# Performance work log

Hardware: AMD Instinct MI355X
Metric: run time of the kernel (lower is better)

The kernel has to match this reference:

```python
import jax, jax.numpy as jnp
import numpy as np

B, S, D_MODEL, N_HEADS, D_HEAD = 2, 2048, 2048, 16, 128


def _rope_tables(seq_len, d_head, base=10000.0):
    # standard llama RoPE cos/sin tables, broadcastable to (B, H, S, d_head)
    inv_freq = 1.0 / (base ** (np.arange(0, d_head, 2, dtype=np.float32) / d_head))
    t = np.arange(seq_len, dtype=np.float32)
    freqs = np.outer(t, inv_freq)                      # (S, d_head/2)
    emb = np.concatenate([freqs, freqs], axis=-1)       # (S, d_head)
    cos = jnp.asarray(np.cos(emb))[None, None]          # (1,1,S,d_head)
    sin = jnp.asarray(np.sin(emb))[None, None]
    return cos, sin


def setup_inputs() -> dict:
    key = jax.random.key(0)
    ks = jax.random.split(key, 5)
    scale = 0.02
    x = jax.random.normal(ks[0], (B, S, D_MODEL), dtype=jnp.float32)
    Wq = jax.random.normal(ks[1], (D_MODEL, D_MODEL), dtype=jnp.float32) * scale
    Wk = jax.random.normal(ks[2], (D_MODEL, D_MODEL), dtype=jnp.float32) * scale
    Wv = jax.random.normal(ks[3], (D_MODEL, D_MODEL), dtype=jnp.float32) * scale
    Wo = jax.random.normal(ks[4], (D_MODEL, D_MODEL), dtype=jnp.float32) * scale
    cos, sin = _rope_tables(S, D_HEAD)
    return {"x": x, "cos": cos, "sin": sin, "Wq": Wq, "Wk": Wk, "Wv": Wv, "Wo": Wo}


def _rotate_half(x):
    x1, x2 = jnp.split(x, 2, axis=-1)
    return jnp.concatenate([-x2, x1], axis=-1)


def _apply_rope(x, cos, sin):
    return x * cos + _rotate_half(x) * sin


def reference(x, cos, sin, Wq, Wk, Wv, Wo):
    b, s, _ = x.shape
    # QKV projections (nn.Linear computes x @ W.T), reshape to (B, H, S, Dh)
    def proj(W):
        return (x @ W.T).reshape(b, s, N_HEADS, D_HEAD).transpose(0, 2, 1, 3)
    q = _apply_rope(proj(Wq), cos, sin)
    k = _apply_rope(proj(Wk), cos, sin)
    v = proj(Wv)
    # causal scaled dot-product attention
    scale = 1.0 / jnp.sqrt(jnp.asarray(D_HEAD, dtype=x.dtype))
    scores = jnp.einsum("bhqd,bhkd->bhqk", q, k) * scale
    causal = jnp.tril(jnp.ones((s, s), dtype=bool))
    scores = jnp.where(causal, scores, jnp.asarray(-jnp.inf, dtype=scores.dtype))
    attn = jax.nn.softmax(scores, axis=-1)
    vals = jnp.einsum("bhqk,bhkd->bhqd", attn, v)
    vals = vals.transpose(0, 2, 1, 3).reshape(b, s, D_MODEL)
    return vals @ Wo.T
```

## Files before the change

### kernel.cpp

```cpp
#include <hip/hip_runtime.h>

#define S_LEN 2048
#define DMODEL 2048
#define NHEADS 16
#define DHEAD 128
#define BATCH 2

typedef unsigned short u16;
typedef __attribute__((ext_vector_type(8))) __bf16 bf16x8;
typedef __attribute__((ext_vector_type(4))) float f32x4;

__device__ __forceinline__ u16 f2bf(float f) {
    union { float f; unsigned int u; } a; a.f = f;
    unsigned int u = a.u;
    u += 0x7fffu + ((u >> 16) & 1u);
    return (u16)(u >> 16);
}
__device__ __forceinline__ u16 f2bf_fast(float f) {
    union { float f; unsigned int u; } a; a.f = f;
    return (u16)((a.u + 0x8000u) >> 16);
}
__device__ __forceinline__ float bf2f(u16 b) {
    union { unsigned int u; float f; } a; a.u = ((unsigned int)b) << 16;
    return a.f;
}

__device__ __forceinline__ void g2l16(const void* g, void* l) {
    __builtin_amdgcn_global_load_lds((const __attribute__((address_space(1))) unsigned int*)g,
                                     (__attribute__((address_space(3))) unsigned int*)l,
                                     16, 0, 0);
}

__global__ void cvt_all(const float* __restrict__ x,
                        const float* __restrict__ w0, const float* __restrict__ w1,
                        const float* __restrict__ w2, const float* __restrict__ w3,
                        u16* __restrict__ xb, u16* __restrict__ wdst) {
    int y = blockIdx.y;
    const float* src;
    u16* out;
    int n4;
    if (y == 0) { src = x; out = xb; n4 = (BATCH * S_LEN * DMODEL) / 4; }
    else {
        src = (y == 1) ? w0 : (y == 2) ? w1 : (y == 3) ? w2 : w3;
        out = wdst + (size_t)(y - 1) * DMODEL * DMODEL;
        n4 = (DMODEL * DMODEL) / 4;
    }
    int i = blockIdx.x * 256 + threadIdx.x;
    if (i >= n4) return;
    f32x4 v = *(const f32x4*)(src + (size_t)i * 4);
    ushort4 o;
    o.x = f2bf(v[0]); o.y = f2bf(v[1]); o.z = f2bf(v[2]); o.w = f2bf(v[3]);
    *(ushort4*)(out + (size_t)i * 4) = o;
}

#define QK_PRESCALE 0.12751744f
__global__ void rope_kernel(u16* __restrict__ Q, u16* __restrict__ K,
                            const float* __restrict__ cosT, const float* __restrict__ sinT) {
    u16* T = blockIdx.z ? K : Q;
    const float pre = blockIdx.z ? 1.0f : QK_PRESCALE;
    int bh = blockIdx.y;
    int t = blockIdx.x * 256 + threadIdx.x;
    int s = t >> 4;
    int d4 = (t & 15) * 4;
    u16* row = T + ((size_t)bh * S_LEN + s) * DHEAD;
    ushort4 lo = *(ushort4*)&row[d4];
    ushort4 hi = *(ushort4*)&row[d4 + 64];
    f32x4 cv = *(const f32x4*)&cosT[s * DHEAD + d4];
    f32x4 sv = *(const f32x4*)&sinT[s * DHEAD + d4];
    float l0 = bf2f(lo.x), l1 = bf2f(lo.y), l2 = bf2f(lo.z), l3 = bf2f(lo.w);
    float h0 = bf2f(hi.x), h1 = bf2f(hi.y), h2 = bf2f(hi.z), h3 = bf2f(hi.w);
    ushort4 olo, ohi;
    olo.x = f2bf((l0 * cv[0] - h0 * sv[0]) * pre);
    olo.y = f2bf((l1 * cv[1] - h1 * sv[1]) * pre);
    olo.z = f2bf((l2 * cv[2] - h2 * sv[2]) * pre);
    olo.w = f2bf((l3 * cv[3] - h3 * sv[3]) * pre);
    ohi.x = f2bf((h0 * cv[0] + l0 * sv[0]) * pre);
    ohi.y = f2bf((h1 * cv[1] + l1 * sv[1]) * pre);
    ohi.z = f2bf((h2 * cv[2] + l2 * sv[2]) * pre);
    ohi.w = f2bf((h3 * cv[3] + l3 * sv[3]) * pre);
    *(ushort4*)&row[d4]      = olo;
    *(ushort4*)&row[d4 + 64] = ohi;
}

__global__ __launch_bounds__(256) void gemm_qkv(const u16* __restrict__ A,
                                                const u16* __restrict__ W,
                                                u16* __restrict__ Qo,
                                                u16* __restrict__ Ko,
                                                u16* __restrict__ Vto) {
    __shared__ u16 As[128 * 32];
    __shared__ u16 Ws[128 * 32];
    const int tid  = threadIdx.x;
    const int lane = tid & 63;
    const int wave = tid >> 6;
    const int wm = wave >> 1, wn = wave & 1;
    const int col = lane & 15, quad = lane >> 4;
    const int blk = blockIdx.x;
    const int xcd = blk & 7;
    const int loc = blk >> 3;
    const int nb  = xcd * 6 + loc % 6;
    const int mb  = loc / 6;
    const int m0 = mb * 128, n0 = nb * 128;
    const int K = DMODEL;
    const int which = n0 >> 11;

    const u16* P0 = (which == 2) ? A : W;
    const u16* P1 = (which == 2) ? W : A;
    const int  r0 = (which == 2) ? m0 : n0;
    const int  r1 = (which == 2) ? n0 : m0;

    f32x4 acc[4][4] = {};

    const int swl = (quad ^ ((col >> 1) & 3)) * 8;
    int a_off[4], w_off[4];
    #pragma unroll
    for (int mi = 0; mi < 4; ++mi) a_off[mi] = (wm * 64 + mi * 16 + col) * 32 + swl;
    #pragma unroll
    for (int ni = 0; ni < 4; ++ni) w_off[ni] = (wn * 64 + ni * 16 + col) * 32 + swl;

    for (int kk = 0; kk < K; kk += 32) {
        #pragma unroll
        for (int i = 0; i < 2; ++i) {
            int c = i * 256 + tid;
            int row = c >> 2;
            int ko = (((c & 3) ^ ((c >> 3) & 3))) * 8;
            int cb = i * 256 + wave * 64;
            g2l16(P0 + (size_t)(r0 + row) * K + kk + ko, (void*)(As + cb * 8));
            g2l16(P1 + (size_t)(r1 + row) * K + kk + ko, (void*)(Ws + cb * 8));
        }
        __syncthreads();
        bf16x8 af[4], wf[4];
        #pragma unroll
        for (int mi = 0; mi < 4; ++mi) af[mi] = *(const bf16x8*)&As[a_off[mi]];
        #pragma unroll
        for (int ni = 0; ni < 4; ++ni) wf[ni] = *(const bf16x8*)&Ws[w_off[ni]];
        #pragma unroll
        for (int mi = 0; mi < 4; ++mi)
            #pragma unroll
            for (int ni = 0; ni < 4; ++ni)
                acc[mi][ni] = __builtin_amdgcn_mfma_f32_16x16x32_bf16(af[mi], wf[ni], acc[mi][ni], 0, 0, 0);
        __syncthreads();
    }

    if (which == 2) {
        #pragma unroll
        for (int mi = 0; mi < 4; ++mi) {
            #pragma unroll
            for (int ni = 0; ni < 4; ++ni) {
                int s0   = m0 + wm * 64 + mi * 16 + quad * 4;
                int ncol = (n0 & 2047) + wn * 64 + ni * 16 + col;
                int b = s0 >> 11, s = s0 & 2047;
                int h = ncol >> 7, d = ncol & 127;
                ushort4 o;
                o.x = f2bf(acc[mi][ni][0]); o.y = f2bf(acc[mi][ni][1]);
                o.z = f2bf(acc[mi][ni][2]); o.w = f2bf(acc[mi][ni][3]);
                *(ushort4*)&Vto[(((size_t)(b * NHEADS + h)) * DHEAD + d) * S_LEN + s] = o;
            }
        }
    } else {
        u16* out = which ? Ko : Qo;
        #pragma unroll
        for (int mi = 0; mi < 4; ++mi) {
            #pragma unroll
            for (int ni = 0; ni < 4; ++ni) {
                int dd = (n0 & 2047) + wm * 64 + mi * 16 + quad * 4;
                int sg = m0 + wn * 64 + ni * 16 + col;
                int b = sg >> 11, s = sg & 2047;
                int h = dd >> 7, d = dd & 127;
                ushort4 o;
                o.x = f2bf(acc[mi][ni][0]); o.y = f2bf(acc[mi][ni][1]);
                o.z = f2bf(acc[mi][ni][2]); o.w = f2bf(acc[mi][ni][3]);
                *(ushort4*)&out[(((size_t)(b * NHEADS + h)) * S_LEN + s) * DHEAD + d] = o;
            }
        }
    }
}

__global__ __launch_bounds__(256) void gemm_out(const u16* __restrict__ A,
                                                const u16* __restrict__ W,
                                                float* __restrict__ out) {
    __shared__ u16 As[128 * 32];
    __shared__ u16 Ws[128 * 32];
    const int tid  = threadIdx.x;
    const int lane = tid & 63;
    const int wave = tid >> 6;
    const int wm = wave >> 1, wn = wave & 1;
    const int col = lane & 15, quad = lane >> 4;
    const int blk = blockIdx.x;
    const int xcd = blk & 7;
    const int loc = blk >> 3;
    const int nb  = xcd * 2 + (loc & 1);
    const int mb  = loc >> 1;
    const int m0 = mb * 128, n0 = nb * 128;
    const int K = DMODEL;

    f32x4 acc[4][4] = {};

    const int swl = (quad ^ ((col >> 1) & 3)) * 8;
    int a_off[4], w_off[4];
    #pragma unroll
    for (int mi = 0; mi < 4; ++mi) a_off[mi] = (wm * 64 + mi * 16 + col) * 32 + swl;
    #pragma unroll
    for (int ni = 0; ni < 4; ++ni) w_off[ni] = (wn * 64 + ni * 16 + col) * 32 + swl;

    for (int kk = 0; kk < K; kk += 32) {
        #pragma unroll
        for (int i = 0; i < 2; ++i) {
            int c = i * 256 + tid;
            int row = c >> 2;
            int ko = (((c & 3) ^ ((c >> 3) & 3))) * 8;
            int cb = i * 256 + wave * 64;
            g2l16(A + (size_t)(m0 + row) * K + kk + ko, (void*)(As + cb * 8));
            g2l16(W + (size_t)(n0 + row) * K + kk + ko, (void*)(Ws + cb * 8));
        }
        __syncthreads();
        bf16x8 af[4], wf[4];
        #pragma unroll
        for (int mi = 0; mi < 4; ++mi) af[mi] = *(const bf16x8*)&As[a_off[mi]];
        #pragma unroll
        for (int ni = 0; ni < 4; ++ni) wf[ni] = *(const bf16x8*)&Ws[w_off[ni]];
        #pragma unroll
        for (int mi = 0; mi < 4; ++mi)
            #pragma unroll
            for (int ni = 0; ni < 4; ++ni)
                acc[mi][ni] = __builtin_amdgcn_mfma_f32_16x16x32_bf16(af[mi], wf[ni], acc[mi][ni], 0, 0, 0);
        __syncthreads();
    }

    #pragma unroll
    for (int mi = 0; mi < 4; ++mi)
        #pragma unroll
        for (int ni = 0; ni < 4; ++ni)
            #pragma unroll
            for (int r = 0; r < 4; ++r) {
                int row  = m0 + wm * 64 + mi * 16 + quad * 4 + r;
                int ncol = n0 + wn * 64 + ni * 16 + col;
                out[(size_t)row * DMODEL + ncol] = acc[mi][ni][r];
            }
}

__global__ __launch_bounds__(256) void attn_kernel(const u16* __restrict__ Q,
                                                   const u16* __restrict__ K,
                                                   const u16* __restrict__ Vt,
                                                   u16* __restrict__ Ao) {
    __shared__ u16 Ks[32 * 136];
    __shared__ u16 Vs[128 * 40];
    __shared__ u16 Ps[4][16 * 40];

    const int tid  = threadIdx.x;
    const int lane = tid & 63;
    const int wave = tid >> 6;
    const int col = lane & 15, quad = lane >> 4;
    const int xcd = blockIdx.x & 7;
    const int sub = (blockIdx.x >> 3) & 3;
    const int bh  = xcd * 4 + sub;
    const int qtile = 31 - (int)(blockIdx.x >> 5);
    const int b = bh >> 4, h = bh & 15;
    const int qb = qtile * 64;
    const int qw = qb + wave * 16;

    const u16* Qb = Q  + (size_t)bh * S_LEN * DHEAD;
    const u16* Kb = K  + (size_t)bh * S_LEN * DHEAD;
    const u16* Vb = Vt + (size_t)bh * DHEAD * S_LEN;

    bf16x8 qf[4];
    #pragma unroll
    for (int dc = 0; dc < 4; ++dc)
        qf[dc] = *(const bf16x8*)&Qb[(size_t)(qw + col) * DHEAD + dc * 32 + quad * 8];

    f32x4 accO[8] = {};
    float lrow = 0.0f;

    const int kend = qb + 64;
    for (int kb = 0; kb < kend; kb += 32) {
        #pragma unroll
        for (int i = 0; i < 2; ++i) {
            int c = tid + i * 256;
            int kr = c >> 4, ko = (c & 15) * 8;
            *(f32x4*)&Ks[kr * 136 + ko] = *(const f32x4*)&Kb[(size_t)(kb + kr) * DHEAD + ko];
            int vr = c >> 2, vo = (c & 3) * 8;
            *(f32x4*)&Vs[vr * 40 + vo] = *(const f32x4*)&Vb[(size_t)vr * S_LEN + kb + vo];
        }
        __syncthreads();

        if (kb <= qw + 15) {
            f32x4 sc[2] = {};
            #pragma unroll
            for (int t = 0; t < 2; ++t)
                #pragma unroll
                for (int dc = 0; dc < 4; ++dc) {
                    bf16x8 kf = *(const bf16x8*)&Ks[(t * 16 + col) * 136 + dc * 32 + quad * 8];
                    sc[t] = __builtin_amdgcn_mfma_f32_16x16x32_bf16(kf, qf[dc], sc[t], 0, 0, 0);
                }

            const int q_g = qw + col;
            float p[2][4];
            #pragma unroll
            for (int t = 0; t < 2; ++t)
                #pragma unroll
                for (int r = 0; r < 4; ++r) {
                    int k_g = kb + t * 16 + quad * 4 + r;
                    float e = exp2f(sc[t][r]);
                    p[t][r] = (k_g <= q_g) ? e : 0.0f;
                    lrow += p[t][r];
                }

            u16* P = Ps[wave];
            #pragma unroll
            for (int t = 0; t < 2; ++t) {
                ushort4 o;
                o.x = f2bf_fast(p[t][0]); o.y = f2bf_fast(p[t][1]);
                o.z = f2bf_fast(p[t][2]); o.w = f2bf_fast(p[t][3]);
                *(ushort4*)&P[col * 40 + t * 16 + quad * 4] = o;
            }
            asm volatile("s_waitcnt lgkmcnt(0)" ::: "memory");
            bf16x8 pf = *(const bf16x8*)&P[col * 40 + quad * 8];

            #pragma unroll
            for (int ni = 0; ni < 8; ++ni) {
                bf16x8 vf = *(const bf16x8*)&Vs[(ni * 16 + col) * 40 + quad * 8];
                accO[ni] = __builtin_amdgcn_mfma_f32_16x16x32_bf16(pf, vf, accO[ni], 0, 0, 0);
            }
        }
        __syncthreads();
    }

    lrow += __shfl_xor(lrow, 16);
    lrow += __shfl_xor(lrow, 32);
    float lb[4];
    #pragma unroll
    for (int r = 0; r < 4; ++r)
        lb[r] = 1.0f / __shfl(lrow, quad * 4 + r);
    #pragma unroll
    for (int ni = 0; ni < 8; ++ni)
        #pragma unroll
        for (int r = 0; r < 4; ++r) {
            int q_g = qw + quad * 4 + r;
            int d = ni * 16 + col;
            Ao[((size_t)(b * S_LEN + q_g)) * DMODEL + h * DHEAD + d] = f2bf(accO[ni][r] * lb[r]);
        }
}

extern "C" void kernel_launch(void* const* d_in, const int* in_sizes, int n_in,
                              void* d_out, int out_size, void* d_ws, size_t ws_size,
                              hipStream_t stream) {
    const float* x    = (const float*)d_in[0];
    const float* cosT = (const float*)d_in[1];
    const float* sinT = (const float*)d_in[2];
    const float* Wq   = (const float*)d_in[3];
    const float* Wk   = (const float*)d_in[4];
    const float* Wv   = (const float*)d_in[5];
    const float* Wo   = (const float*)d_in[6];

    char* ws = (char*)d_ws;
    size_t off = 0;
    auto carve = [&](size_t bytes) {
        void* p = ws + off;
        off += (bytes + 255) & ~(size_t)255;
        return p;
    };
    const size_t xN = (size_t)BATCH * S_LEN * DMODEL;
    const size_t wN = (size_t)DMODEL * DMODEL;
    u16* xb   = (u16*)carve(xN * 2);
    u16* wqkv = (u16*)carve(wN * 2 * 4);
    u16* wob  = wqkv + wN * 3;
    u16* Qb   = (u16*)carve(xN * 2);
    u16* Kb   = (u16*)carve(xN * 2);
    u16* Vtb  = (u16*)carve(xN * 2);
    u16* attn = xb;

    cvt_all<<<dim3(8192, 5), 256, 0, stream>>>(x, Wq, Wk, Wv, Wo, xb, wqkv);

    gemm_qkv<<<dim3(1536), 256, 0, stream>>>(xb, wqkv, Qb, Kb, Vtb);

    rope_kernel<<<dim3(S_LEN * 16 / 256, BATCH * NHEADS, 2), 256, 0, stream>>>(Qb, Kb, cosT, sinT);

    attn_kernel<<<dim3(1024), 256, 0, stream>>>(Qb, Kb, Vtb, attn);

    gemm_out<<<dim3(512), 256, 0, stream>>>(attn, wob, (float*)d_out);
}
```

Baseline: 401.6 us.

## Rewrite projection GEMMs with 128x256 tiles and triple-buffered async LDS pipeline

Both projection GEMMs now share one core that uses 512-thread blocks with 128x256 output tiles and BK=64. Tiles are staged into a three-deep LDS ring with direct global-to-LDS loads and partial vmcnt waits, so loads for tile t+2 overlap the MFMA work on tile t and one barrier per step replaces two. MFMA phases are raised in priority with setprio, and the block-to-tile mapping is remapped per XCD. The cost is much more shared memory per block (about 144 KB) and fewer, larger blocks, which lowers occupancy and makes the waves harder to balance.

```diff
diff --git a/kernel.cpp b/kernel.cpp
--- a/kernel.cpp
+++ b/kernel.cpp
@@ -5,6 +5,8 @@
 #define NHEADS 16
 #define DHEAD 128
 #define BATCH 2
+#define BK 64
+#define NT (DMODEL / BK)
 
 typedef unsigned short u16;
 typedef __attribute__((ext_vector_type(8))) __bf16 bf16x8;
@@ -82,88 +84,132 @@
     *(ushort4*)&row[d4 + 64] = ohi;
 }
 
-__global__ __launch_bounds__(256) void gemm_qkv(const u16* __restrict__ A,
-                                                const u16* __restrict__ W,
-                                                u16* __restrict__ Qo,
-                                                u16* __restrict__ Ko,
-                                                u16* __restrict__ Vto) {
-    __shared__ u16 As[128 * 32];
-    __shared__ u16 Ws[128 * 32];
-    const int tid  = threadIdx.x;
-    const int lane = tid & 63;
-    const int wave = tid >> 6;
-    const int wm = wave >> 1, wn = wave & 1;
+
+__device__ __forceinline__ void stage_a(const u16* __restrict__ P, int r0, int kk,
+                                        u16* dst, int tid) {
+    #pragma unroll
+    for (int i = 0; i < 2; ++i) {
+        int n = i * 512 + tid;
+        int row = (n >> 2) & 127;
+        int ks  = n >> 9;
+        int x   = n & 3;
+        g2l16(P + (size_t)(r0 + row) * DMODEL + kk + ks * 32 + ((x ^ ((row >> 1) & 3)) * 8),
+              (void*)(dst + (i * 512 + (tid >> 6) * 64) * 8));
+    }
+}
+
+__device__ __forceinline__ void stage_b(const u16* __restrict__ P, int r0, int kk,
+                                        u16* dst, int tid) {
+    #pragma unroll
+    for (int i = 0; i < 4; ++i) {
+        int n = i * 512 + tid;
+        int row = (n >> 2) & 255;
+        int ks  = n >> 10;
+        int x   = n & 3;
+        g2l16(P + (size_t)(r0 + row) * DMODEL + kk + ks * 32 + ((x ^ ((row >> 1) & 3)) * 8),
+              (void*)(dst + (i * 512 + (tid >> 6) * 64) * 8));
+    }
+}
+
+__device__ __forceinline__ void gemm_core(const u16* __restrict__ Aop, int a0,
+                                          const u16* __restrict__ Bop, int b0,
+                                          u16* As, u16* Ws,
+                                          f32x4 (&acc)[4][4], int tid) {
+    const int lane = tid & 63, wave = tid >> 6;
+    const int wm = wave >> 2, wn = wave & 3;
     const int col = lane & 15, quad = lane >> 4;
-    const int blk = blockIdx.x;
-    const int xcd = blk & 7;
-    const int loc = blk >> 3;
-    const int nb  = xcd * 6 + loc % 6;
-    const int mb  = loc / 6;
-    const int m0 = mb * 128, n0 = nb * 128;
-    const int K = DMODEL;
-    const int which = n0 >> 11;
-
-    const u16* P0 = (which == 2) ? A : W;
-    const u16* P1 = (which == 2) ? W : A;
-    const int  r0 = (which == 2) ? m0 : n0;
-    const int  r1 = (which == 2) ? n0 : m0;
+    const int swl = (quad ^ ((col >> 1) & 3)) * 8;
+
+    stage_a(Aop, a0, 0, As, tid);
+    stage_b(Bop, b0, 0, Ws, tid);
+    stage_a(Aop, a0, BK, As + 8192, tid);
+    stage_b(Bop, b0, BK, Ws + 16384, tid);
+
+    int a_off[4], w_off[4];
+    #pragma unroll
+    for (int mi = 0; mi < 4; ++mi) a_off[mi] = (wm * 64 + mi * 16 + col) * 32 + swl;
+    #pragma unroll
+    for (int ni = 0; ni < 4; ++ni) w_off[ni] = (wn * 64 + ni * 16 + col) * 32 + swl;
+
+    asm volatile("s_waitcnt vmcnt(6)" ::: "memory");
+    __builtin_amdgcn_s_barrier();
+
+    int pc = 0, ps = 2;
+    for (int t = 0; t < NT; ++t) {
+        if (t + 2 < NT) {
+            stage_a(Aop, a0, (t + 2) * BK, As + ps * 8192, tid);
+            stage_b(Bop, b0, (t + 2) * BK, Ws + ps * 16384, tid);
+            ps = (ps == 2) ? 0 : ps + 1;
+        }
+        const u16* Ab = As + pc * 8192;
+        const u16* Wb = Ws + pc * 16384;
+        pc = (pc == 2) ? 0 : pc + 1;
+
+        bf16x8 af[4][2], wf[4][2];
+        #pragma unroll
+        for (int ks = 0; ks < 2; ++ks) {
+            #pragma unroll
+            for (int mi = 0; mi < 4; ++mi) af[mi][ks] = *(const bf16x8*)&Ab[ks * 4096 + a_off[mi]];
+            #pragma unroll
+            for (int ni = 0; ni < 4; ++ni) wf[ni][ks] = *(const bf16x8*)&Wb[ks * 8192 + w_off[ni]];
+        }
+        __builtin_amdgcn_s_setprio(1);
+        #pragma unroll
+        for (int ks = 0; ks < 2; ++ks)
+            #pragma unroll
+            for (int mi = 0; mi < 4; ++mi)
+                #pragma unroll
+                for (int ni = 0; ni < 4; ++ni)
+                    acc[mi][ni] = __builtin_amdgcn_mfma_f32_16x16x32_bf16(af[mi][ks], wf[ni][ks], acc[mi][ni], 0, 0, 0);
+        __builtin_amdgcn_s_setprio(0);
+        __builtin_amdgcn_sched_barrier(0);
+        if (t + 1 < NT) {
+            if (t + 2 < NT) { asm volatile("s_waitcnt vmcnt(6)" ::: "memory"); }
+            else            { asm volatile("s_waitcnt vmcnt(0)" ::: "memory"); }
+            __builtin_amdgcn_s_barrier();
+        }
+    }
+}
+
+__global__ __launch_bounds__(512, 2) void gemm_qkv(const u16* __restrict__ A,
+                                                   const u16* __restrict__ W,
+                                                   u16* __restrict__ Qo,
+                                                   u16* __restrict__ Ko,
+                                                   u16* __restrict__ Vto) {
+    __shared__ u16 As[3 * 8192];
+    __shared__ u16 Ws[3 * 16384];
+    const int tid = threadIdx.x;
+    const int orig = blockIdx.x;
+    const int blk = (orig & 7) * 96 + (orig >> 3);
+    const int region = blk >> 8;
+    const int local  = blk & 255;
+
+    const u16* Aop; const u16* Bop; int a0, b0;
+    if (region < 2) {
+        a0 = region * 2048 + (local & 15) * 128;
+        b0 = (local >> 4) * 256;
+        Aop = W; Bop = A;
+    } else {
+        a0 = (local & 31) * 128;
+        b0 = 4096 + (local >> 5) * 256;
+        Aop = A; Bop = W;
+    }
 
     f32x4 acc[4][4] = {};
-
-    const int swl = (quad ^ ((col >> 1) & 3)) * 8;
-    int a_off[4], w_off[4];
-    #pragma unroll
-    for (int mi = 0; mi < 4; ++mi) a_off[mi] = (wm * 64 + mi * 16 + col) * 32 + swl;
-    #pragma unroll
-    for (int ni = 0; ni < 4; ++ni) w_off[ni] = (wn * 64 + ni * 16 + col) * 32 + swl;
-
-    for (int kk = 0; kk < K; kk += 32) {
-        #pragma unroll
-        for (int i = 0; i < 2; ++i) {
-            int c = i * 256 + tid;
-            int row = c >> 2;
-            int ko = (((c & 3) ^ ((c >> 3) & 3))) * 8;
-            int cb = i * 256 + wave * 64;
-            g2l16(P0 + (size_t)(r0 + row) * K + kk + ko, (void*)(As + cb * 8));
-            g2l16(P1 + (size_t)(r1 + row) * K + kk + ko, (void*)(Ws + cb * 8));
-        }
-        __syncthreads();
-        bf16x8 af[4], wf[4];
-        #pragma unroll
-        for (int mi = 0; mi < 4; ++mi) af[mi] = *(const bf16x8*)&As[a_off[mi]];
-        #pragma unroll
-        for (int ni = 0; ni < 4; ++ni) wf[ni] = *(const bf16x8*)&Ws[w_off[ni]];
+    gemm_core(Aop, a0, Bop, b0, As, Ws, acc, tid);
+
+    const int lane = tid & 63, wave = tid >> 6;
+    const int wm = wave >> 2, wn = wave & 3;
+    const int col = lane & 15, quad = lane >> 4;
+
+    if (region < 2) {
+        u16* out = region ? Ko : Qo;
         #pragma unroll
         for (int mi = 0; mi < 4; ++mi)
             #pragma unroll
-            for (int ni = 0; ni < 4; ++ni)
-                acc[mi][ni] = __builtin_amdgcn_mfma_f32_16x16x32_bf16(af[mi], wf[ni], acc[mi][ni], 0, 0, 0);
-        __syncthreads();
-    }
-
-    if (which == 2) {
-        #pragma unroll
-        for (int mi = 0; mi < 4; ++mi) {
-            #pragma unroll
             for (int ni = 0; ni < 4; ++ni) {
-                int s0   = m0 + wm * 64 + mi * 16 + quad * 4;
-                int ncol = (n0 & 2047) + wn * 64 + ni * 16 + col;
-                int b = s0 >> 11, s = s0 & 2047;
-                int h = ncol >> 7, d = ncol & 127;
-                ushort4 o;
-                o.x = f2bf(acc[mi][ni][0]); o.y = f2bf(acc[mi][ni][1]);
-                o.z = f2bf(acc[mi][ni][2]); o.w = f2bf(acc[mi][ni][3]);
-                *(ushort4*)&Vto[(((size_t)(b * NHEADS + h)) * DHEAD + d) * S_LEN + s] = o;
-            }
-        }
-    } else {
-        u16* out = which ? Ko : Qo;
-        #pragma unroll
-        for (int mi = 0; mi < 4; ++mi) {
-            #pragma unroll
-            for (int ni = 0; ni < 4; ++ni) {
-                int dd = (n0 & 2047) + wm * 64 + mi * 16 + quad * 4;
-                int sg = m0 + wn * 64 + ni * 16 + col;
+                int dd = (a0 & 2047) + wm * 64 + mi * 16 + quad * 4;
+                int sg = b0 + wn * 64 + ni * 16 + col;
                 int b = sg >> 11, s = sg & 2047;
                 int h = dd >> 7, d = dd & 127;
                 ushort4 o;
@@ -171,61 +217,40 @@
                 o.z = f2bf(acc[mi][ni][2]); o.w = f2bf(acc[mi][ni][3]);
                 *(ushort4*)&out[(((size_t)(b * NHEADS + h)) * S_LEN + s) * DHEAD + d] = o;
             }
-        }
-    }
-}
-
-__global__ __launch_bounds__(256) void gemm_out(const u16* __restrict__ A,
-                                                const u16* __restrict__ W,
-                                                float* __restrict__ out) {
-    __shared__ u16 As[128 * 32];
-    __shared__ u16 Ws[128 * 32];
-    const int tid  = threadIdx.x;
-    const int lane = tid & 63;
-    const int wave = tid >> 6;
-    const int wm = wave >> 1, wn = wave & 1;
+    } else {
+        #pragma unroll
+        for (int mi = 0; mi < 4; ++mi)
+            #pragma unroll
+            for (int ni = 0; ni < 4; ++ni) {
+                int s0 = a0 + wm * 64 + mi * 16 + quad * 4;
+                int nc = (b0 - 4096) + wn * 64 + ni * 16 + col;
+                int b = s0 >> 11, s = s0 & 2047;
+                int h = nc >> 7, d = nc & 127;
+                ushort4 o;
+                o.x = f2bf(acc[mi][ni][0]); o.y = f2bf(acc[mi][ni][1]);
+                o.z = f2bf(acc[mi][ni][2]); o.w = f2bf(acc[mi][ni][3]);
+                *(ushort4*)&Vto[(((size_t)(b * NHEADS + h)) * DHEAD + d) * S_LEN + s] = o;
+            }
+    }
+}
+
+__global__ __launch_bounds__(512, 2) void gemm_out(const u16* __restrict__ A,
+                                                   const u16* __restrict__ W,
+                                                   float* __restrict__ out) {
+    __shared__ u16 As[3 * 8192];
+    __shared__ u16 Ws[3 * 16384];
+    const int tid = threadIdx.x;
+    const int orig = blockIdx.x;
+    const int blk = (orig & 7) * 32 + (orig >> 3);
+    const int m0 = (blk & 31) * 128;
+    const int n0 = (blk >> 5) * 256;
+
+    f32x4 acc[4][4] = {};
+    gemm_core(A, m0, W, n0, As, Ws, acc, tid);
+
+    const int lane = tid & 63, wave = tid >> 6;
+    const int wm = wave >> 2, wn = wave & 3;
     const int col = lane & 15, quad = lane >> 4;
-    const int blk = blockIdx.x;
-    const int xcd = blk & 7;
-    const int loc = blk >> 3;
-    const int nb  = xcd * 2 + (loc & 1);
-    const int mb  = loc >> 1;
-    const int m0 = mb * 128, n0 = nb * 128;
-    const int K = DMODEL;
-
-    f32x4 acc[4][4] = {};
-
-    const int swl = (quad ^ ((col >> 1) & 3)) * 8;
-    int a_off[4], w_off[4];
-    #pragma unroll
-    for (int mi = 0; mi < 4; ++mi) a_off[mi] = (wm * 64 + mi * 16 + col) * 32 + swl;
-    #pragma unroll
-    for (int ni = 0; ni < 4; ++ni) w_off[ni] = (wn * 64 + ni * 16 + col) * 32 + swl;
-
-    for (int kk = 0; kk < K; kk += 32) {
-        #pragma unroll
-        for (int i = 0; i < 2; ++i) {
-            int c = i * 256 + tid;
-            int row = c >> 2;
-            int ko = (((c & 3) ^ ((c >> 3) & 3))) * 8;
-            int cb = i * 256 + wave * 64;
-            g2l16(A + (size_t)(m0 + row) * K + kk + ko, (void*)(As + cb * 8));
-            g2l16(W + (size_t)(n0 + row) * K + kk + ko, (void*)(Ws + cb * 8));
-        }
-        __syncthreads();
-        bf16x8 af[4], wf[4];
-        #pragma unroll
-        for (int mi = 0; mi < 4; ++mi) af[mi] = *(const bf16x8*)&As[a_off[mi]];
-        #pragma unroll
-        for (int ni = 0; ni < 4; ++ni) wf[ni] = *(const bf16x8*)&Ws[w_off[ni]];
-        #pragma unroll
-        for (int mi = 0; mi < 4; ++mi)
-            #pragma unroll
-            for (int ni = 0; ni < 4; ++ni)
-                acc[mi][ni] = __builtin_amdgcn_mfma_f32_16x16x32_bf16(af[mi], wf[ni], acc[mi][ni], 0, 0, 0);
-        __syncthreads();
-    }
-
     #pragma unroll
     for (int mi = 0; mi < 4; ++mi)
         #pragma unroll
@@ -370,11 +395,11 @@
 
     cvt_all<<<dim3(8192, 5), 256, 0, stream>>>(x, Wq, Wk, Wv, Wo, xb, wqkv);
 
-    gemm_qkv<<<dim3(1536), 256, 0, stream>>>(xb, wqkv, Qb, Kb, Vtb);
+    gemm_qkv<<<dim3(768), 512, 0, stream>>>(xb, wqkv, Qb, Kb, Vtb);
 
     rope_kernel<<<dim3(S_LEN * 16 / 256, BATCH * NHEADS, 2), 256, 0, stream>>>(Qb, Kb, cosT, sinT);
 
     attn_kernel<<<dim3(1024), 256, 0, stream>>>(Qb, Kb, Vtb, attn);
 
-    gemm_out<<<dim3(512), 256, 0, stream>>>(attn, wob, (float*)d_out);
-}
+    gemm_out<<<dim3(256), 512, 0, stream>>>(attn, wob, (float*)d_out);
+}
```

After: 442.5 us. 10.2% more time.

## Triple-buffer LDS tiles in projection GEMMs with async prefetch two stages ahead

Applied to the files above, without the earlier changes.

Both projection GEMMs now share a core loop that keeps three LDS buffers and issues direct global-to-LDS loads for tile t+2 while tile t runs. It waits with vmcnt counters and uses one barrier per iteration instead of two, so the load latency that the old load-sync-compute-sync loop exposed can overlap with MFMA work. It also raises wave priority around the MFMA block. In exchange LDS use triples to 48 KB per block, which can lower occupancy, and the counter-based waits are fragile if the load count per stage changes.

```diff
diff --git a/kernel.cpp b/kernel.cpp
--- a/kernel.cpp
+++ b/kernel.cpp
@@ -5,6 +5,8 @@
 #define NHEADS 16
 #define DHEAD 128
 #define BATCH 2
+#define BK 32
+#define NT (DMODEL / BK)
 
 typedef unsigned short u16;
 typedef __attribute__((ext_vector_type(8))) __bf16 bf16x8;
@@ -82,25 +84,87 @@
     *(ushort4*)&row[d4 + 64] = ohi;
 }
 
+
+__device__ __forceinline__ void stage32(const u16* __restrict__ Aop, int r0a,
+                                        const u16* __restrict__ Bop, int r0b,
+                                        int kk, u16* Abuf, u16* Wbuf, int tid) {
+    #pragma unroll
+    for (int i = 0; i < 2; ++i) {
+        int c = i * 256 + tid;
+        int row = c >> 2;
+        int ko = (((c & 3) ^ ((c >> 3) & 3))) * 8;
+        int cb = (i * 256 + (tid >> 6) * 64) * 8;
+        g2l16(Aop + (size_t)(r0a + row) * DMODEL + kk + ko, (void*)(Abuf + cb));
+        g2l16(Bop + (size_t)(r0b + row) * DMODEL + kk + ko, (void*)(Wbuf + cb));
+    }
+}
+
+__device__ __forceinline__ void gemm_core(const u16* __restrict__ Aop, int a0,
+                                          const u16* __restrict__ Bop, int b0,
+                                          u16* As, u16* Ws,
+                                          f32x4 (&acc)[4][4], int tid) {
+    const int lane = tid & 63, wave = tid >> 6;
+    const int wm = wave >> 1, wn = wave & 1;
+    const int col = lane & 15, quad = lane >> 4;
+    const int swl = (quad ^ ((col >> 1) & 3)) * 8;
+
+    int a_off[4], w_off[4];
+    #pragma unroll
+    for (int mi = 0; mi < 4; ++mi) a_off[mi] = (wm * 64 + mi * 16 + col) * 32 + swl;
+    #pragma unroll
+    for (int ni = 0; ni < 4; ++ni) w_off[ni] = (wn * 64 + ni * 16 + col) * 32 + swl;
+
+    stage32(Aop, a0, Bop, b0, 0, As, Ws, tid);
+    stage32(Aop, a0, Bop, b0, BK, As + 4096, Ws + 4096, tid);
+
+    asm volatile("s_waitcnt vmcnt(4)" ::: "memory");
+    __builtin_amdgcn_s_barrier();
+
+    int pc = 0, ps = 2;
+    for (int t = 0; t < NT; ++t) {
+        if (t + 2 < NT) {
+            stage32(Aop, a0, Bop, b0, (t + 2) * BK, As + ps * 4096, Ws + ps * 4096, tid);
+            ps = (ps == 2) ? 0 : ps + 1;
+        }
+        const u16* Ab = As + pc * 4096;
+        const u16* Wb = Ws + pc * 4096;
+        pc = (pc == 2) ? 0 : pc + 1;
+
+        bf16x8 af[4], wf[4];
+        #pragma unroll
+        for (int mi = 0; mi < 4; ++mi) af[mi] = *(const bf16x8*)&Ab[a_off[mi]];
+        #pragma unroll
+        for (int ni = 0; ni < 4; ++ni) wf[ni] = *(const bf16x8*)&Wb[w_off[ni]];
+        __builtin_amdgcn_s_setprio(1);
+        #pragma unroll
+        for (int mi = 0; mi < 4; ++mi)
+            #pragma unroll
+            for (int ni = 0; ni < 4; ++ni)
+                acc[mi][ni] = __builtin_amdgcn_mfma_f32_16x16x32_bf16(af[mi], wf[ni], acc[mi][ni], 0, 0, 0);
+        __builtin_amdgcn_s_setprio(0);
+        __builtin_amdgcn_sched_barrier(0);
+        if (t + 1 < NT) {
+            if (t + 2 < NT) { asm volatile("s_waitcnt vmcnt(4)" ::: "memory"); }
+            else            { asm volatile("s_waitcnt vmcnt(0)" ::: "memory"); }
+            __builtin_amdgcn_s_barrier();
+        }
+    }
+}
+
 __global__ __launch_bounds__(256) void gemm_qkv(const u16* __restrict__ A,
                                                 const u16* __restrict__ W,
                                                 u16* __restrict__ Qo,
                                                 u16* __restrict__ Ko,
                                                 u16* __restrict__ Vto) {
-    __shared__ u16 As[128 * 32];
-    __shared__ u16 Ws[128 * 32];
+    __shared__ u16 As[3 * 4096];
+    __shared__ u16 Ws[3 * 4096];
     const int tid  = threadIdx.x;
-    const int lane = tid & 63;
-    const int wave = tid >> 6;
-    const int wm = wave >> 1, wn = wave & 1;
-    const int col = lane & 15, quad = lane >> 4;
     const int blk = blockIdx.x;
     const int xcd = blk & 7;
     const int loc = blk >> 3;
     const int nb  = xcd * 6 + loc % 6;
     const int mb  = loc / 6;
     const int m0 = mb * 128, n0 = nb * 128;
-    const int K = DMODEL;
     const int which = n0 >> 11;
 
     const u16* P0 = (which == 2) ? A : W;
@@ -109,37 +173,11 @@
     const int  r1 = (which == 2) ? n0 : m0;
 
     f32x4 acc[4][4] = {};
-
-    const int swl = (quad ^ ((col >> 1) & 3)) * 8;
-    int a_off[4], w_off[4];
-    #pragma unroll
-    for (int mi = 0; mi < 4; ++mi) a_off[mi] = (wm * 64 + mi * 16 + col) * 32 + swl;
-    #pragma unroll
-    for (int ni = 0; ni < 4; ++ni) w_off[ni] = (wn * 64 + ni * 16 + col) * 32 + swl;
-
-    for (int kk = 0; kk < K; kk += 32) {
-        #pragma unroll
-        for (int i = 0; i < 2; ++i) {
-            int c = i * 256 + tid;
-            int row = c >> 2;
-            int ko = (((c & 3) ^ ((c >> 3) & 3))) * 8;
-            int cb = i * 256 + wave * 64;
-            g2l16(P0 + (size_t)(r0 + row) * K + kk + ko, (void*)(As + cb * 8));
-            g2l16(P1 + (size_t)(r1 + row) * K + kk + ko, (void*)(Ws + cb * 8));
-        }
-        __syncthreads();
-        bf16x8 af[4], wf[4];
-        #pragma unroll
-        for (int mi = 0; mi < 4; ++mi) af[mi] = *(const bf16x8*)&As[a_off[mi]];
-        #pragma unroll
-        for (int ni = 0; ni < 4; ++ni) wf[ni] = *(const bf16x8*)&Ws[w_off[ni]];
-        #pragma unroll
-        for (int mi = 0; mi < 4; ++mi)
-            #pragma unroll
-            for (int ni = 0; ni < 4; ++ni)
-                acc[mi][ni] = __builtin_amdgcn_mfma_f32_16x16x32_bf16(af[mi], wf[ni], acc[mi][ni], 0, 0, 0);
-        __syncthreads();
-    }
+    gemm_core(P0, r0, P1, r1, As, Ws, acc, tid);
+
+    const int lane = tid & 63, wave = tid >> 6;
+    const int wm = wave >> 1, wn = wave & 1;
+    const int col = lane & 15, quad = lane >> 4;
 
     if (which == 2) {
         #pragma unroll
@@ -178,54 +216,22 @@
 __global__ __launch_bounds__(256) void gemm_out(const u16* __restrict__ A,
                                                 const u16* __restrict__ W,
                                                 float* __restrict__ out) {
-    __shared__ u16 As[128 * 32];
-    __shared__ u16 Ws[128 * 32];
+    __shared__ u16 As[3 * 4096];
+    __shared__ u16 Ws[3 * 4096];
     const int tid  = threadIdx.x;
-    const int lane = tid & 63;
-    const int wave = tid >> 6;
-    const int wm = wave >> 1, wn = wave & 1;
-    const int col = lane & 15, quad = lane >> 4;
     const int blk = blockIdx.x;
     const int xcd = blk & 7;
     const int loc = blk >> 3;
     const int nb  = xcd * 2 + (loc & 1);
     const int mb  = loc >> 1;
     const int m0 = mb * 128, n0 = nb * 128;
-    const int K = DMODEL;
 
     f32x4 acc[4][4] = {};
-
-    const int swl = (quad ^ ((col >> 1) & 3)) * 8;
-    int a_off[4], w_off[4];
-    #pragma unroll
-    for (int mi = 0; mi < 4; ++mi) a_off[mi] = (wm * 64 + mi * 16 + col) * 32 + swl;
-    #pragma unroll
-    for (int ni = 0; ni < 4; ++ni) w_off[ni] = (wn * 64 + ni * 16 + col) * 32 + swl;
-
-    for (int kk = 0; kk < K; kk += 32) {
-        #pragma unroll
-        for (int i = 0; i < 2; ++i) {
-            int c = i * 256 + tid;
-            int row = c >> 2;
-            int ko = (((c & 3) ^ ((c >> 3) & 3))) * 8;
-            int cb = i * 256 + wave * 64;
-            g2l16(A + (size_t)(m0 + row) * K + kk + ko, (void*)(As + cb * 8));
-            g2l16(W + (size_t)(n0 + row) * K + kk + ko, (void*)(Ws + cb * 8));
-        }
-        __syncthreads();
-        bf16x8 af[4], wf[4];
-        #pragma unroll
-        for (int mi = 0; mi < 4; ++mi) af[mi] = *(const bf16x8*)&As[a_off[mi]];
-        #pragma unroll
-        for (int ni = 0; ni < 4; ++ni) wf[ni] = *(const bf16x8*)&Ws[w_off[ni]];
-        #pragma unroll
-        for (int mi = 0; mi < 4; ++mi)
-            #pragma unroll
-            for (int ni = 0; ni < 4; ++ni)
-                acc[mi][ni] = __builtin_amdgcn_mfma_f32_16x16x32_bf16(af[mi], wf[ni], acc[mi][ni], 0, 0, 0);
-        __syncthreads();
-    }
-
+    gemm_core(A, m0, W, n0, As, Ws, acc, tid);
+
+    const int lane = tid & 63, wave = tid >> 6;
+    const int wm = wave >> 1, wn = wave & 1;
+    const int col = lane & 15, quad = lane >> 4;
     #pragma unroll
     for (int mi = 0; mi < 4; ++mi)
         #pragma unroll
```

Result: slower. 430.3 us (+7.1%).
